# Kernel tuning notes

Measured on AMD Instinct MI355X. Metric: run time of the kernel, lower is better.

## Reference

```python
import jax, jax.numpy as jnp
import numpy as np
import math

NUM_HEADS = 8
NUM_CHANNELS = 512
B, C, H, W = 8, 512, 32, 32
LN_EPS = 1e-6


def setup_inputs() -> dict:
    key = jax.random.key(0)
    ks = jax.random.split(key, 7)
    s = 1.0 / math.sqrt(NUM_CHANNELS)
    return {
        "key": jax.random.normal(ks[0], (B, C, H, W), jnp.float32),
        "value": jax.random.normal(ks[1], (B, C, H, W), jnp.float32),
        "query": jax.random.normal(ks[2], (B, C, H, W), jnp.float32),
        "Wq": jax.random.normal(ks[3], (C, C), jnp.float32) * s,
        "Wk": jax.random.normal(ks[4], (C, C), jnp.float32) * s,
        "Wv": jax.random.normal(ks[5], (C, C), jnp.float32) * s,
        "Wo": jax.random.normal(ks[6], (C, C), jnp.float32) * s,
        "ln_gamma": jnp.ones((C,), jnp.float32),
        "ln_beta": jnp.zeros((C,), jnp.float32),
    }


def _to_tokens(x):
    # b c h w -> b (h w) c
    b, c, h, w = x.shape
    return x.transpose(0, 2, 3, 1).reshape(b, h * w, c)


def _split_heads(x, m):
    # (B, HW, C) -> (B, m, HW, d); matches reshape (B,HW,m,d) then 'b hw m d -> (b m) hw d'
    b, hw, c = x.shape
    d = c // m
    return x.reshape(b, hw, m, d).transpose(0, 2, 1, 3)


def _merge_heads_cm(x):
    # (B, m, HW, d) -> (B, HW, d*m) with channel index = c*m + head  ('(b m) hw c -> b hw (c m)')
    b, m, hw, d = x.shape
    return x.transpose(0, 2, 3, 1).reshape(b, hw, d * m)


def reference(key, value, query, Wq, Wk, Wv, Wo, ln_gamma, ln_beta):
    m = NUM_HEADS
    b, c, h, w = query.shape
    d = c // m

    q = _to_tokens(query) @ Wq.T  # (B, HW, C)
    k = _to_tokens(key) @ Wk.T
    v = _to_tokens(value) @ Wv.T

    qh = _split_heads(q, m)  # (B, m, HW, d)
    kh = _split_heads(k, m)
    vh = _split_heads(v, m)

    scores = jnp.einsum('bmqd,bmkd->bmqk', qh, kh) / math.sqrt(d)
    p_attn = jax.nn.softmax(scores, axis=-1)
    out = jnp.einsum('bmqk,bmkd->bmqd', p_attn, vh)  # (B, m, HW, d)

    out = _merge_heads_cm(out)        # (B, HW, C) interleaved as (c m)
    residual = _merge_heads_cm(qh)    # same interleaving of projected query

    x = out + residual
    mu = jnp.mean(x, axis=-1, keepdims=True)
    var = jnp.mean(jnp.square(x - mu), axis=-1, keepdims=True)
    x = (x - mu) / jnp.sqrt(var + LN_EPS) * ln_gamma + ln_beta

    x = x @ Wo.T  # (B, HW, C)
    return x.reshape(b, h, w, c).transpose(0, 3, 1, 2)  # b (h w) c -> b c h w
```

## Files before the change

kernel.cpp:

```cpp
#include <hip/hip_runtime.h>
#include <stdint.h>

typedef __bf16 bf16x8 __attribute__((ext_vector_type(8)));
typedef float f32x4 __attribute__((ext_vector_type(4)));
typedef unsigned short u16x4 __attribute__((ext_vector_type(4)));
typedef unsigned short u16x8 __attribute__((ext_vector_type(8)));

#define MFMA16(a, b, c) __builtin_amdgcn_mfma_f32_16x16x32_bf16(a, b, c, 0, 0, 0)

__device__ __forceinline__ unsigned short f2bf(float f) {
  union { float f; unsigned u; } v; v.f = f;
  unsigned r = v.u + 0x7fffu + ((v.u >> 16) & 1u);
  return (unsigned short)(r >> 16);
}
__device__ __forceinline__ float bf2f(unsigned short h) {
  union { unsigned u; float f; } v; v.u = ((unsigned)h) << 16; return v.f;
}
__device__ __forceinline__ unsigned pk2(float a, float b) {
  union { unsigned u; __bf16 h[2]; } v;
  v.h[0] = (__bf16)a;
  v.h[1] = (__bf16)b;
  return v.u;
}
__device__ __forceinline__ void gload16(const void* g, void* l) {
  __builtin_amdgcn_global_load_lds(
      (const __attribute__((address_space(1))) void*)g,
      (__attribute__((address_space(3))) void*)l, 16, 0, 0);
}
__device__ __forceinline__ float fexp2(float x) {
#if __has_builtin(__builtin_amdgcn_exp2f)
  return __builtin_amdgcn_exp2f(x);
#else
  return exp2f(x);
#endif
}

__global__ __launch_bounds__(256) void prep_kernel(
    const float* __restrict__ q, const float* __restrict__ k,
    const float* __restrict__ v, unsigned short* __restrict__ oq,
    unsigned short* __restrict__ ok, unsigned short* __restrict__ ov,
    const float* __restrict__ w0, const float* __restrict__ w1,
    const float* __restrict__ w2, const float* __restrict__ w3,
    unsigned short* __restrict__ y0, unsigned short* __restrict__ y1,
    unsigned short* __restrict__ y2, unsigned short* __restrict__ y3) {
  __shared__ float tile[64][33];
  int z = blockIdx.z;
  if (z == 3) {
    int idx = blockIdx.y * 32 + blockIdx.x;
    if (idx >= 512) return;
    int wsel = idx >> 7, xb = idx & 127;
    const float* s = wsel == 0 ? w0 : wsel == 1 ? w1 : wsel == 2 ? w2 : w3;
    unsigned short* d = wsel == 0 ? y0 : wsel == 1 ? y1 : wsel == 2 ? y2 : y3;
    int t = xb * 256 + threadIdx.x;
    const f32x4* sp = (const f32x4*)(s + (size_t)t * 8);
    f32x4 a = sp[0], b = sp[1];
    u16x8 r;
    r[0] = f2bf(a[0]); r[1] = f2bf(a[1]); r[2] = f2bf(a[2]); r[3] = f2bf(a[3]);
    r[4] = f2bf(b[0]); r[5] = f2bf(b[1]); r[6] = f2bf(b[2]); r[7] = f2bf(b[3]);
    *(u16x8*)(d + (size_t)t * 8) = r;
    return;
  }
  const float* src = z == 0 ? q : z == 1 ? k : v;
  unsigned short* dst = z == 0 ? oq : z == 1 ? ok : ov;
  int bb = blockIdx.y >> 3;
  int c0 = (blockIdx.y & 7) * 64;
  int t0 = blockIdx.x * 32;
  int tx = threadIdx.x & 31, r = threadIdx.x >> 5;
#pragma unroll
  for (int i = 0; i < 8; ++i)
    tile[r + i * 8][tx] = src[(size_t)(bb * 512 + c0 + r + i * 8) * 1024 + t0 + tx];
  __syncthreads();
#pragma unroll
  for (int i = 0; i < 4; ++i) {
    int tr = r + i * 8;
    unsigned pack = (unsigned)f2bf(tile[2 * tx][tr]) |
                    ((unsigned)f2bf(tile[2 * tx + 1][tr]) << 16);
    *(unsigned*)(dst + (size_t)(bb * 1024 + t0 + tr) * 512 + c0 + 2 * tx) = pack;
  }
}

__global__ __launch_bounds__(256, 4) void gemm_qkv(
    const unsigned short* __restrict__ A0, const unsigned short* __restrict__ A1,
    const unsigned short* __restrict__ A2,
    const unsigned short* __restrict__ B0, const unsigned short* __restrict__ B1,
    const unsigned short* __restrict__ B2,
    unsigned short* __restrict__ O0, unsigned short* __restrict__ O1,
    unsigned short* __restrict__ O2) {
  __shared__ unsigned short aT[2][128 * 32];
  __shared__ unsigned short bT[2][128 * 32];
  int z = blockIdx.y;
  const unsigned short* A = z == 0 ? A0 : z == 1 ? A1 : A2;
  const unsigned short* BT = z == 0 ? B0 : z == 1 ? B1 : B2;
  int j = blockIdx.x;
  int bm = (j & 7) * 8 + (j >> 5);
  int bn = (j >> 3) & 3;
  int tid = threadIdx.x, lane = tid & 63, w = tid >> 6;
  int wr = w >> 1, wc = w & 1, l15 = lane & 15, lhi = lane >> 4;
  const int m0 = bm * 128, n0 = bn * 128;

  int u0 = tid, u1 = 256 + tid;
  int ar0 = u0 >> 2, ac0 = (u0 & 3) ^ (ar0 & 3);
  int ar1 = u1 >> 2, ac1 = (u1 & 3) ^ (ar1 & 3);
  const unsigned short* asrc0 = A + (size_t)(m0 + ar0) * 512 + ac0 * 8;
  const unsigned short* asrc1 = A + (size_t)(m0 + ar1) * 512 + ac1 * 8;
  const unsigned short* bsrc0 = BT + (size_t)(n0 + ar0) * 512 + ac0 * 8;
  const unsigned short* bsrc1 = BT + (size_t)(n0 + ar1) * 512 + ac1 * 8;

#define QSTAGE(bufi, it)                                     \
  do {                                                       \
    gload16(asrc0 + (it) * 32, &aT[bufi][u0 * 8]);           \
    gload16(asrc1 + (it) * 32, &aT[bufi][u1 * 8]);           \
    gload16(bsrc0 + (it) * 32, &bT[bufi][u0 * 8]);           \
    gload16(bsrc1 + (it) * 32, &bT[bufi][u1 * 8]);           \
  } while (0)

  int aoff[4], boff[4];
#pragma unroll
  for (int i = 0; i < 4; ++i) {
    int arow = wr * 64 + i * 16 + l15;
    int brow = wc * 64 + i * 16 + l15;
    aoff[i] = arow * 32 + ((lhi ^ (arow & 3)) * 8);
    boff[i] = brow * 32 + ((lhi ^ (brow & 3)) * 8);
  }

  f32x4 acc[4][4] = {};

#define QTILE(BUF, IT)                                                        \
  do {                                                                       \
    if ((IT) + 1 < 16) QSTAGE((BUF) ^ 1, (IT) + 1);                           \
    bf16x8 af[4], bfr[4];                                                    \
    _Pragma("unroll") for (int mi = 0; mi < 4; ++mi)                          \
        af[mi] = *(const bf16x8*)&aT[BUF][aoff[mi]];                          \
    _Pragma("unroll") for (int ni = 0; ni < 4; ++ni)                          \
        bfr[ni] = *(const bf16x8*)&bT[BUF][boff[ni]];                         \
    __builtin_amdgcn_s_setprio(1);                                           \
    _Pragma("unroll") for (int mi = 0; mi < 4; ++mi)                          \
        _Pragma("unroll") for (int ni = 0; ni < 4; ++ni)                      \
            acc[mi][ni] = MFMA16(af[mi], bfr[ni], acc[mi][ni]);               \
    __builtin_amdgcn_s_setprio(0);                                           \
    __syncthreads();                                                         \
  } while (0)

  QSTAGE(0, 0);
  __syncthreads();
  for (int it2 = 0; it2 < 16; it2 += 2) {
    QTILE(0, it2);
    QTILE(1, it2 + 1);
  }
#undef QTILE
#undef QSTAGE

  float sc = (z == 1) ? (0.125f * 1.44269504f) : 1.0f;
#pragma unroll
  for (int mi = 0; mi < 4; ++mi) {
#pragma unroll
    for (int ni = 0; ni < 4; ++ni) {
      int row = m0 + wr * 64 + mi * 16 + lhi * 4;
      int col = n0 + wc * 64 + ni * 16 + l15;
      if (z < 2) {
        unsigned short* C = z == 0 ? O0 : O1;
#pragma unroll
        for (int j2 = 0; j2 < 4; ++j2)
          C[(size_t)(row + j2) * 512 + col] = f2bf(acc[mi][ni][j2] * sc);
      } else {
        int bb = row >> 10, hw = row & 1023;
        u16x4 p;
        p[0] = f2bf(acc[mi][ni][0]); p[1] = f2bf(acc[mi][ni][1]);
        p[2] = f2bf(acc[mi][ni][2]); p[3] = f2bf(acc[mi][ni][3]);
        *(u16x4*)&O2[(size_t)bb * 524288 + (size_t)col * 1024 + hw] = p;
      }
    }
  }
}

__global__ __launch_bounds__(256, 4) void gemm_out(const unsigned short* __restrict__ A,
                                                   const unsigned short* __restrict__ BT,
                                                   float* __restrict__ C) {
  __shared__ unsigned short aT[2][128 * 32];
  __shared__ unsigned short bT[2][64 * 32];
  int j = blockIdx.x;
  int bm = (j & 7) * 8 + (j >> 6);
  int bn = (j >> 3) & 7;
  int tid = threadIdx.x, lane = tid & 63, w = tid >> 6;
  int l15 = lane & 15, lhi = lane >> 4;
  const int m0 = bm * 128, n0 = bn * 64;

  int u0 = tid, u1 = 256 + tid;
  int ar0 = u0 >> 2, ac0 = (u0 & 3) ^ (ar0 & 3);
  int ar1 = u1 >> 2, ac1 = (u1 & 3) ^ (ar1 & 3);
  const unsigned short* asrc0 = A + (size_t)(m0 + ar0) * 512 + ac0 * 8;
  const unsigned short* asrc1 = A + (size_t)(m0 + ar1) * 512 + ac1 * 8;
  const unsigned short* bsrc0 = BT + (size_t)(n0 + ar0) * 512 + ac0 * 8;

#define OSTAGE(bufi, it)                                     \
  do {                                                       \
    gload16(asrc0 + (it) * 32, &aT[bufi][u0 * 8]);           \
    gload16(asrc1 + (it) * 32, &aT[bufi][u1 * 8]);           \
    gload16(bsrc0 + (it) * 32, &bT[bufi][u0 * 8]);           \
  } while (0)

  int aoff[2], boff[4];
#pragma unroll
  for (int i = 0; i < 2; ++i) {
    int arow = w * 32 + i * 16 + l15;
    aoff[i] = arow * 32 + ((lhi ^ (arow & 3)) * 8);
  }
#pragma unroll
  for (int i = 0; i < 4; ++i) {
    int brow = i * 16 + l15;
    boff[i] = brow * 32 + ((lhi ^ (brow & 3)) * 8);
  }

  f32x4 acc[2][4] = {};

#define OTILE(BUF, IT)                                                        \
  do {                                                                       \
    if ((IT) + 1 < 16) OSTAGE((BUF) ^ 1, (IT) + 1);                           \
    bf16x8 af[2], bfr[4];                                                    \
    _Pragma("unroll") for (int mi = 0; mi < 2; ++mi)                          \
        af[mi] = *(const bf16x8*)&aT[BUF][aoff[mi]];                          \
    _Pragma("unroll") for (int ni = 0; ni < 4; ++ni)                          \
        bfr[ni] = *(const bf16x8*)&bT[BUF][boff[ni]];                         \
    __builtin_amdgcn_s_setprio(1);                                           \
    _Pragma("unroll") for (int mi = 0; mi < 2; ++mi)                          \
        _Pragma("unroll") for (int ni = 0; ni < 4; ++ni)                      \
            acc[mi][ni] = MFMA16(af[mi], bfr[ni], acc[mi][ni]);               \
    __builtin_amdgcn_s_setprio(0);                                           \
    __syncthreads();                                                         \
  } while (0)

  OSTAGE(0, 0);
  __syncthreads();
  for (int it2 = 0; it2 < 16; it2 += 2) {
    OTILE(0, it2);
    OTILE(1, it2 + 1);
  }
#undef OTILE
#undef OSTAGE

#pragma unroll
  for (int mi = 0; mi < 2; ++mi) {
#pragma unroll
    for (int ni = 0; ni < 4; ++ni) {
      int row = m0 + w * 32 + mi * 16 + lhi * 4;
      int col = n0 + ni * 16 + l15;
      int bb = row >> 10, hw = row & 1023;
      *(f32x4*)&C[(size_t)bb * 524288 + (size_t)col * 1024 + hw] = acc[mi][ni];
    }
  }
}

__global__ __launch_bounds__(256, 4) void attn_kernel(
    const unsigned short* __restrict__ q_tok, const unsigned short* __restrict__ k_tok,
    const unsigned short* __restrict__ v_cm, unsigned short* __restrict__ y_hm) {
  __shared__ unsigned short k_lds[2][64 * 64];
  __shared__ unsigned short v_lds[2][64 * 64];
  __shared__ unsigned short p_lds[4][16 * 64];

  int bid = blockIdx.x;
  int slot = bid >> 3;
  int bh = (bid & 7) * 8 + (slot >> 4);
  int qb = slot & 15;
  int h = bh & 7, b = bh >> 3;
  int tid = threadIdx.x;
  int lane = tid & 63, w = tid >> 6;
  int l15 = lane & 15, lhi = lane >> 4;

  const unsigned short* kbase = k_tok + (size_t)b * 524288 + h * 64;
  const unsigned short* vbase = v_cm + (size_t)b * 524288 + (size_t)h * 65536;

  int qglob0 = b * 1024 + qb * 64 + w * 16;
  const unsigned short* qp = q_tok + (size_t)(qglob0 + l15) * 512 + h * 64 + lhi * 8;
  bf16x8 qf0 = *(const bf16x8*)qp;
  bf16x8 qf1 = *(const bf16x8*)(qp + 32);

  bf16x8 ones;
#pragma unroll
  for (int i = 0; i < 8; ++i) ones[i] = (__bf16)1.0f;

  int u0 = tid, u1 = 256 + tid;
  int r0 = u0 >> 3, c0 = (u0 & 7) ^ (r0 & 7);
  int r1 = u1 >> 3, c1 = (u1 & 7) ^ (r1 & 7);
  const unsigned short* ksrc0 = kbase + (size_t)r0 * 512 + c0 * 8;
  const unsigned short* ksrc1 = kbase + (size_t)r1 * 512 + c1 * 8;
  const unsigned short* vsrc0 = vbase + (size_t)r0 * 1024 + c0 * 8;
  const unsigned short* vsrc1 = vbase + (size_t)r1 * 1024 + c1 * 8;

#define STAGE(bufi, kti)                                                    \
  do {                                                                      \
    gload16(ksrc0 + (size_t)(kti) * 32768, &k_lds[bufi][u0 * 8]);           \
    gload16(ksrc1 + (size_t)(kti) * 32768, &k_lds[bufi][u1 * 8]);           \
    gload16(vsrc0 + (kti) * 64, &v_lds[bufi][u0 * 8]);                      \
    gload16(vsrc1 + (kti) * 64, &v_lds[bufi][u1 * 8]);                      \
  } while (0)

  int kvoff[4][2];
#pragma unroll
  for (int nt = 0; nt < 4; ++nt) {
    int brow = nt * 16 + l15, sw = brow & 7;
    kvoff[nt][0] = brow * 64 + ((lhi ^ sw) * 8);
    kvoff[nt][1] = brow * 64 + (((4 + lhi) ^ sw) * 8);
  }

  char* pb = (char*)&p_lds[w][0];
  int p2 = (l15 & 7) << 1;
  char* pwr[4];
  const char* prd[2];
#pragma unroll
  for (int nt = 0; nt < 4; ++nt)
    pwr[nt] = pb + l15 * 128 + ((((nt << 2) | lhi) ^ p2) << 3);
#pragma unroll
  for (int kc = 0; kc < 2; ++kc)
    prd[kc] = pb + l15 * 128 + ((((kc << 3) | (lhi << 1)) ^ p2) << 3);

  f32x4 ls = {0.f, 0.f, 0.f, 0.f};
  f32x4 o[4] = {};

#define TILE(BUF, KT)                                                        \
  do {                                                                       \
    if ((KT) + 1 < 16) STAGE((BUF) ^ 1, (KT) + 1);                           \
    const unsigned short* kl = k_lds[BUF];                                   \
    const unsigned short* vl = v_lds[BUF];                                   \
    f32x4 st[4];                                                             \
    __builtin_amdgcn_s_setprio(1);                                           \
    _Pragma("unroll") for (int nt = 0; nt < 4; ++nt) {                       \
      bf16x8 kf0 = *(const bf16x8*)&kl[kvoff[nt][0]];                        \
      bf16x8 kf1 = *(const bf16x8*)&kl[kvoff[nt][1]];                        \
      f32x4 a = {0.f, 0.f, 0.f, 0.f};                                        \
      a = MFMA16(kf0, qf0, a);                                               \
      a = MFMA16(kf1, qf1, a);                                               \
      st[nt] = a;                                                            \
    }                                                                        \
    __builtin_amdgcn_s_setprio(0);                                           \
    bf16x8 vf[4][2];                                                         \
    _Pragma("unroll") for (int dt = 0; dt < 4; ++dt) {                       \
      vf[dt][0] = *(const bf16x8*)&vl[kvoff[dt][0]];                         \
      vf[dt][1] = *(const bf16x8*)&vl[kvoff[dt][1]];                         \
    }                                                                        \
    _Pragma("unroll") for (int nt = 0; nt < 4; ++nt) {                       \
      float e0 = fexp2(st[nt][0]);                                           \
      float e1 = fexp2(st[nt][1]);                                           \
      float e2 = fexp2(st[nt][2]);                                           \
      float e3 = fexp2(st[nt][3]);                                           \
      uint2 pk;                                                              \
      pk.x = pk2(e0, e1);                                                    \
      pk.y = pk2(e2, e3);                                                    \
      *(uint2*)pwr[nt] = pk;                                                 \
    }                                                                        \
    asm volatile("" ::: "memory");                                          \
    bf16x8 pf0 = *(const bf16x8*)prd[0];                                     \
    bf16x8 pf1 = *(const bf16x8*)prd[1];                                     \
    __builtin_amdgcn_s_setprio(1);                                           \
    _Pragma("unroll") for (int dt = 0; dt < 4; ++dt) {                       \
      o[dt] = MFMA16(pf0, vf[dt][0], o[dt]);                                 \
      o[dt] = MFMA16(pf1, vf[dt][1], o[dt]);                                 \
    }                                                                        \
    ls = MFMA16(pf0, ones, ls);                                              \
    ls = MFMA16(pf1, ones, ls);                                              \
    __builtin_amdgcn_s_setprio(0);                                           \
    __syncthreads();                                                         \
  } while (0)

  STAGE(0, 0);
  __syncthreads();
  for (int kt2 = 0; kt2 < 16; kt2 += 2) {
    TILE(0, kt2);
    TILE(1, kt2 + 1);
  }
#undef TILE
#undef STAGE

  float inv[4];
#pragma unroll
  for (int r = 0; r < 4; ++r) inv[r] = 1.0f / ls[r];
#pragma unroll
  for (int dt = 0; dt < 4; ++dt) {
#pragma unroll
    for (int r = 0; r < 4; ++r) {
      int q = qglob0 + lhi * 4 + r;
      size_t idx = (size_t)q * 512 + h * 64 + dt * 16 + l15;
      float res = bf2f(q_tok[idx]);
      y_hm[idx] = f2bf(o[dt][r] * inv[r] + res);
    }
  }
}

__global__ __launch_bounds__(256) void ln_kernel(
    const unsigned short* __restrict__ y_hm,
    const float* __restrict__ gamma, const float* __restrict__ beta,
    unsigned short* __restrict__ xln) {
  __shared__ float y_s[512];
  __shared__ float red[8];
  int row = blockIdx.x;
  int t = threadIdx.x;
  float y0 = bf2f(y_hm[(size_t)row * 512 + t]);
  float y1 = bf2f(y_hm[(size_t)row * 512 + 256 + t]);
  y_s[t] = y0;
  y_s[t + 256] = y1;
  float s = y0 + y1, ss = y0 * y0 + y1 * y1;
#pragma unroll
  for (int msk = 1; msk < 64; msk <<= 1) {
    s += __shfl_xor(s, msk);
    ss += __shfl_xor(ss, msk);
  }
  int w = t >> 6, lane = t & 63;
  if (lane == 0) { red[w] = s; red[4 + w] = ss; }
  __syncthreads();
  s = (red[0] + red[1]) + (red[2] + red[3]);
  ss = (red[4] + red[5]) + (red[6] + red[7]);
  float mean = s * (1.0f / 512.0f);
  float var = ss * (1.0f / 512.0f) - mean * mean;
  float rstd = rsqrtf(var + 1e-6f);
  int c0 = t, c1 = t + 256;
  int p0 = ((c0 & 7) << 6) | (c0 >> 3);
  int p1 = ((c1 & 7) << 6) | (c1 >> 3);
  xln[(size_t)row * 512 + c0] = f2bf((y_s[p0] - mean) * rstd * gamma[c0] + beta[c0]);
  xln[(size_t)row * 512 + c1] = f2bf((y_s[p1] - mean) * rstd * gamma[c1] + beta[c1]);
}

extern "C" void kernel_launch(void* const* d_in, const int* in_sizes, int n_in,
                              void* d_out, int out_size, void* d_ws, size_t ws_size,
                              hipStream_t stream) {
  const float* key   = (const float*)d_in[0];
  const float* value = (const float*)d_in[1];
  const float* query = (const float*)d_in[2];
  const float* Wq = (const float*)d_in[3];
  const float* Wk = (const float*)d_in[4];
  const float* Wv = (const float*)d_in[5];
  const float* Wo = (const float*)d_in[6];
  const float* gamma = (const float*)d_in[7];
  const float* beta  = (const float*)d_in[8];

  char* ws = (char*)d_ws;
  unsigned short* Wq_b = (unsigned short*)(ws);
  unsigned short* Wk_b = Wq_b + 262144;
  unsigned short* Wv_b = Wk_b + 262144;
  unsigned short* Wo_b = Wv_b + 262144;
  unsigned short* qT    = (unsigned short*)(ws + (size_t)(2u)  * 1048576);
  unsigned short* kT    = (unsigned short*)(ws + (size_t)(10u) * 1048576);
  unsigned short* vT    = (unsigned short*)(ws + (size_t)(18u) * 1048576);
  unsigned short* q_tok = (unsigned short*)(ws + (size_t)(26u) * 1048576);
  unsigned short* k_tok = (unsigned short*)(ws + (size_t)(34u) * 1048576);
  unsigned short* v_cm  = (unsigned short*)(ws + (size_t)(42u) * 1048576);
  unsigned short* xln   = qT;
  unsigned short* y_hm  = (unsigned short*)d_out;

  prep_kernel<<<dim3(32, 64, 4), 256, 0, stream>>>(query, key, value, qT, kT, vT,
                                                   Wq, Wk, Wv, Wo,
                                                   Wq_b, Wk_b, Wv_b, Wo_b);
  gemm_qkv<<<dim3(256, 3), 256, 0, stream>>>(qT, kT, vT, Wq_b, Wk_b, Wv_b,
                                             q_tok, k_tok, v_cm);
  attn_kernel<<<1024, 256, 0, stream>>>(q_tok, k_tok, v_cm, y_hm);
  ln_kernel<<<8192, 256, 0, stream>>>(y_hm, gamma, beta, xln);
  gemm_out<<<512, 256, 0, stream>>>(xln, Wo_b, (float*)d_out);
}
```

Measured before the change: 89.74 us.

## Process two query sub-tiles per wave in attention to reuse K/V tiles

Each attention block now covers 128 queries instead of 64, with each wave handling two 16-row query sub-tiles, so every K/V tile staged in LDS feeds twice as many MFMAs. The grid halves to 512 blocks and launch bounds drop to 2 blocks per CU to leave room for the doubled accumulators and P buffers. This cuts global K/V traffic and LDS fragment reads per query, at the cost of more registers, lower occupancy and fewer blocks to fill the GPU.

```diff
diff --git a/kernel.cpp b/kernel.cpp
--- a/kernel.cpp
+++ b/kernel.cpp
@@ -250,17 +250,17 @@
   }
 }
 
-__global__ __launch_bounds__(256, 4) void attn_kernel(
+__global__ __launch_bounds__(256, 2) void attn_kernel(
     const unsigned short* __restrict__ q_tok, const unsigned short* __restrict__ k_tok,
     const unsigned short* __restrict__ v_cm, unsigned short* __restrict__ y_hm) {
   __shared__ unsigned short k_lds[2][64 * 64];
   __shared__ unsigned short v_lds[2][64 * 64];
-  __shared__ unsigned short p_lds[4][16 * 64];
+  __shared__ unsigned short p_lds[4][2][16 * 64];
 
   int bid = blockIdx.x;
   int slot = bid >> 3;
-  int bh = (bid & 7) * 8 + (slot >> 4);
-  int qb = slot & 15;
+  int bh = (bid & 7) * 8 + (slot >> 3);
+  int qb = slot & 7;
   int h = bh & 7, b = bh >> 3;
   int tid = threadIdx.x;
   int lane = tid & 63, w = tid >> 6;
@@ -269,10 +269,15 @@
   const unsigned short* kbase = k_tok + (size_t)b * 524288 + h * 64;
   const unsigned short* vbase = v_cm + (size_t)b * 524288 + (size_t)h * 65536;
 
-  int qglob0 = b * 1024 + qb * 64 + w * 16;
-  const unsigned short* qp = q_tok + (size_t)(qglob0 + l15) * 512 + h * 64 + lhi * 8;
-  bf16x8 qf0 = *(const bf16x8*)qp;
-  bf16x8 qf1 = *(const bf16x8*)(qp + 32);
+  int qglob0 = b * 1024 + qb * 128 + w * 32;
+  bf16x8 qf[2][2];
+#pragma unroll
+  for (int sub = 0; sub < 2; ++sub) {
+    const unsigned short* qp =
+        q_tok + (size_t)(qglob0 + sub * 16 + l15) * 512 + h * 64 + lhi * 8;
+    qf[sub][0] = *(const bf16x8*)qp;
+    qf[sub][1] = *(const bf16x8*)(qp + 32);
+  }
 
   bf16x8 ones;
 #pragma unroll
@@ -302,34 +307,39 @@
     kvoff[nt][1] = brow * 64 + (((4 + lhi) ^ sw) * 8);
   }
 
-  char* pb = (char*)&p_lds[w][0];
+  char* pb = (char*)&p_lds[w][0][0];
   int p2 = (l15 & 7) << 1;
-  char* pwr[4];
-  const char* prd[2];
-#pragma unroll
-  for (int nt = 0; nt < 4; ++nt)
-    pwr[nt] = pb + l15 * 128 + ((((nt << 2) | lhi) ^ p2) << 3);
-#pragma unroll
-  for (int kc = 0; kc < 2; ++kc)
-    prd[kc] = pb + l15 * 128 + ((((kc << 3) | (lhi << 1)) ^ p2) << 3);
-
-  f32x4 ls = {0.f, 0.f, 0.f, 0.f};
-  f32x4 o[4] = {};
+  char* pwr[2][4];
+  const char* prd[2][2];
+#pragma unroll
+  for (int sub = 0; sub < 2; ++sub) {
+#pragma unroll
+    for (int nt = 0; nt < 4; ++nt)
+      pwr[sub][nt] = pb + sub * 2048 + l15 * 128 + ((((nt << 2) | lhi) ^ p2) << 3);
+#pragma unroll
+    for (int kc = 0; kc < 2; ++kc)
+      prd[sub][kc] = pb + sub * 2048 + l15 * 128 + ((((kc << 3) | (lhi << 1)) ^ p2) << 3);
+  }
+
+  f32x4 ls[2] = {{0.f, 0.f, 0.f, 0.f}, {0.f, 0.f, 0.f, 0.f}};
+  f32x4 o[2][4] = {};
 
 #define TILE(BUF, KT)                                                        \
   do {                                                                       \
     if ((KT) + 1 < 16) STAGE((BUF) ^ 1, (KT) + 1);                           \
     const unsigned short* kl = k_lds[BUF];                                   \
     const unsigned short* vl = v_lds[BUF];                                   \
-    f32x4 st[4];                                                             \
+    f32x4 st[2][4];                                                          \
     __builtin_amdgcn_s_setprio(1);                                           \
     _Pragma("unroll") for (int nt = 0; nt < 4; ++nt) {                       \
       bf16x8 kf0 = *(const bf16x8*)&kl[kvoff[nt][0]];                        \
       bf16x8 kf1 = *(const bf16x8*)&kl[kvoff[nt][1]];                        \
-      f32x4 a = {0.f, 0.f, 0.f, 0.f};                                        \
-      a = MFMA16(kf0, qf0, a);                                               \
-      a = MFMA16(kf1, qf1, a);                                               \
-      st[nt] = a;                                                            \
+      _Pragma("unroll") for (int sub = 0; sub < 2; ++sub) {                  \
+        f32x4 a = {0.f, 0.f, 0.f, 0.f};                                      \
+        a = MFMA16(kf0, qf[sub][0], a);                                      \
+        a = MFMA16(kf1, qf[sub][1], a);                                      \
+        st[sub][nt] = a;                                                     \
+      }                                                                      \
     }                                                                        \
     __builtin_amdgcn_s_setprio(0);                                           \
     bf16x8 vf[4][2];                                                         \
@@ -337,26 +347,35 @@
       vf[dt][0] = *(const bf16x8*)&vl[kvoff[dt][0]];                         \
       vf[dt][1] = *(const bf16x8*)&vl[kvoff[dt][1]];                         \
     }                                                                        \
-    _Pragma("unroll") for (int nt = 0; nt < 4; ++nt) {                       \
-      float e0 = fexp2(st[nt][0]);                                           \
-      float e1 = fexp2(st[nt][1]);                                           \
-      float e2 = fexp2(st[nt][2]);                                           \
-      float e3 = fexp2(st[nt][3]);                                           \
-      uint2 pk;                                                              \
-      pk.x = pk2(e0, e1);                                                    \
-      pk.y = pk2(e2, e3);                                                    \
-      *(uint2*)pwr[nt] = pk;                                                 \
+    _Pragma("unroll") for (int sub = 0; sub < 2; ++sub) {                    \
+      _Pragma("unroll") for (int nt = 0; nt < 4; ++nt) {                     \
+        float e0 = fexp2(st[sub][nt][0]);                                    \
+        float e1 = fexp2(st[sub][nt][1]);                                    \
+        float e2 = fexp2(st[sub][nt][2]);                                    \
+        float e3 = fexp2(st[sub][nt][3]);                                    \
+        uint2 pk;                                                            \
+        pk.x = pk2(e0, e1);                                                  \
+        pk.y = pk2(e2, e3);                                                  \
+        *(uint2*)pwr[sub][nt] = pk;                                          \
+      }                                                                      \
     }                                                                        \
     asm volatile("" ::: "memory");                                          \
-    bf16x8 pf0 = *(const bf16x8*)prd[0];                                     \
-    bf16x8 pf1 = *(const bf16x8*)prd[1];                                     \
+    bf16x8 pf[2][2];                                                         \
+    _Pragma("unroll") for (int sub = 0; sub < 2; ++sub) {                    \
+      pf[sub][0] = *(const bf16x8*)prd[sub][0];                              \
+      pf[sub][1] = *(const bf16x8*)prd[sub][1];                              \
+    }                                                                        \
     __builtin_amdgcn_s_setprio(1);                                           \
     _Pragma("unroll") for (int dt = 0; dt < 4; ++dt) {                       \
-      o[dt] = MFMA16(pf0, vf[dt][0], o[dt]);                                 \
-      o[dt] = MFMA16(pf1, vf[dt][1], o[dt]);                                 \
-    }                                                                        \
-    ls = MFMA16(pf0, ones, ls);                                              \
-    ls = MFMA16(pf1, ones, ls);                                              \
+      _Pragma("unroll") for (int sub = 0; sub < 2; ++sub) {                  \
+        o[sub][dt] = MFMA16(pf[sub][0], vf[dt][0], o[sub][dt]);              \
+        o[sub][dt] = MFMA16(pf[sub][1], vf[dt][1], o[sub][dt]);              \
+      }                                                                      \
+    }                                                                        \
+    _Pragma("unroll") for (int sub = 0; sub < 2; ++sub) {                    \
+      ls[sub] = MFMA16(pf[sub][0], ones, ls[sub]);                           \
+      ls[sub] = MFMA16(pf[sub][1], ones, ls[sub]);                           \
+    }                                                                        \
     __builtin_amdgcn_s_setprio(0);                                           \
     __syncthreads();                                                         \
   } while (0)
@@ -370,17 +389,20 @@
 #undef TILE
 #undef STAGE
 
-  float inv[4];
-#pragma unroll
-  for (int r = 0; r < 4; ++r) inv[r] = 1.0f / ls[r];
-#pragma unroll
-  for (int dt = 0; dt < 4; ++dt) {
-#pragma unroll
-    for (int r = 0; r < 4; ++r) {
-      int q = qglob0 + lhi * 4 + r;
-      size_t idx = (size_t)q * 512 + h * 64 + dt * 16 + l15;
-      float res = bf2f(q_tok[idx]);
-      y_hm[idx] = f2bf(o[dt][r] * inv[r] + res);
+#pragma unroll
+  for (int sub = 0; sub < 2; ++sub) {
+    float inv[4];
+#pragma unroll
+    for (int r = 0; r < 4; ++r) inv[r] = 1.0f / ls[sub][r];
+#pragma unroll
+    for (int dt = 0; dt < 4; ++dt) {
+#pragma unroll
+      for (int r = 0; r < 4; ++r) {
+        int q = qglob0 + sub * 16 + lhi * 4 + r;
+        size_t idx = (size_t)q * 512 + h * 64 + dt * 16 + l15;
+        float res = bf2f(q_tok[idx]);
+        y_hm[idx] = f2bf(o[sub][dt][r] * inv[r] + res);
+      }
     }
   }
 }
@@ -450,7 +472,7 @@
                                                    Wq_b, Wk_b, Wv_b, Wo_b);
   gemm_qkv<<<dim3(256, 3), 256, 0, stream>>>(qT, kT, vT, Wq_b, Wk_b, Wv_b,
                                              q_tok, k_tok, v_cm);
-  attn_kernel<<<1024, 256, 0, stream>>>(q_tok, k_tok, v_cm, y_hm);
+  attn_kernel<<<512, 256, 0, stream>>>(q_tok, k_tok, v_cm, y_hm);
   ln_kernel<<<8192, 256, 0, stream>>>(y_hm, gamma, beta, xln);
   gemm_out<<<512, 256, 0, stream>>>(xln, Wo_b, (float*)d_out);
 }
```

After: 87.03 us. 1.03x faster.
